# Kernel optimization log

Measured on AMD Instinct MI355X. Metric: run time of the kernel, lower is better.

Reference implementation:

```python
import jax, jax.numpy as jnp
import numpy as np

B, S, E, H = 2, 2048, 1024, 16
D = E // H  # head_dim = 64
SCALE = D ** -0.5
NEG = -1e9


def setup_inputs() -> dict:
    key = jax.random.key(0)
    ks = jax.random.split(key, 10)
    hidden_states = jax.random.normal(ks[0], (B, S, E), dtype=jnp.float32)
    # CLIP-style additive causal mask [B, 1, L, S]
    causal = jnp.where(jnp.tril(jnp.ones((S, S), dtype=bool)), 0.0, NEG).astype(jnp.float32)
    attn_mask = jnp.broadcast_to(causal, (B, 1, S, S))
    def lin(kw, kb):
        W = jax.random.normal(kw, (E, E), dtype=jnp.float32) * (E ** -0.5)
        b = jax.random.normal(kb, (E,), dtype=jnp.float32) * 0.02
        return W, b
    Wq, bq = lin(ks[1], ks[2])
    Wk, bk = lin(ks[3], ks[4])
    Wv, bv = lin(ks[5], ks[6])
    Wo, bo = lin(ks[7], ks[8])
    return {"hidden_states": hidden_states, "attn_mask": attn_mask,
            "Wq": Wq, "bq": bq, "Wk": Wk, "bk": bk,
            "Wv": Wv, "bv": bv, "Wo": Wo, "bo": bo}


def reference(hidden_states, attn_mask, Wq, bq, Wk, bk, Wv, bv, Wo, bo):
    b, L, e = hidden_states.shape
    # projections (nn.Linear: x @ W.T + b)
    def split_heads(x):
        return x.reshape(b, L, H, D).transpose(0, 2, 1, 3)  # [b,h,l,d]
    q = split_heads(hidden_states @ Wq.T + bq)
    k = split_heads(hidden_states @ Wk.T + bk)
    v = split_heads(hidden_states @ Wv.T + bv)
    # QK^T * scale + additive mask, softmax, AV (dropout_p = 0 in eval)
    scores = jnp.einsum('bhld,bhsd->bhls', q, k) * SCALE + attn_mask
    attn = jax.nn.softmax(scores, axis=-1)
    ctx = jnp.einsum('bhls,bhsd->bhld', attn, v)
    ctx = ctx.transpose(0, 2, 1, 3).reshape(b, L, e)
    return ctx @ Wo.T + bo
```

## Files before the change

### kernel.cpp

```cpp
#include <hip/hip_runtime.h>
#include <hip/hip_bf16.h>
#include <stdint.h>


typedef __hip_bfloat16 bf16;
typedef short bf16x8 __attribute__((ext_vector_type(8)));
typedef short bf16x4 __attribute__((ext_vector_type(4)));
typedef float f32x4 __attribute__((ext_vector_type(4)));

__device__ __forceinline__ f32x4 mfma16(bf16x8 a, bf16x8 b, f32x4 c) {
  return __builtin_amdgcn_mfma_f32_16x16x32_bf16(a, b, c, 0, 0, 0);
}

__device__ __forceinline__ f32x4 mfma_k16(bf16x4 a, bf16x4 b, f32x4 c) {
#if __has_builtin(__builtin_amdgcn_mfma_f32_16x16x16bf16_1k)
  return __builtin_amdgcn_mfma_f32_16x16x16bf16_1k(a, b, c, 0, 0, 0);
#else
  f32x4 d;
  asm volatile("v_mfma_f32_16x16x16_bf16 %0, %1, %2, %3\n\ts_nop 7\n\ts_nop 7"
               : "=v"(d)
               : "v"(a), "v"(b), "v"(c));
  return d;
#endif
}

__device__ __forceinline__ void async16(const void* g, void* l) {
  __builtin_amdgcn_global_load_lds((const __attribute__((address_space(1))) void*)g,
                                   (__attribute__((address_space(3))) void*)l, 16, 0, 0);
}

__global__ __launch_bounds__(256) void cvt_kernel(
    const float* __restrict__ hs, const float* __restrict__ Wq,
    const float* __restrict__ Wk, const float* __restrict__ Wv,
    const float* __restrict__ Wo, bf16* __restrict__ dst) {
  const size_t e = ((size_t)blockIdx.x * 256 + threadIdx.x) * 8;
  const float* src;
  size_t off;
  if (e < 4194304) {
    src = hs; off = e;
  } else {
    const size_t w = e - 4194304;
    const int wi = (int)(w >> 20);
    src = (wi == 0) ? Wq : (wi == 1) ? Wk : (wi == 2) ? Wv : Wo;
    off = w & 1048575;
  }
  const float4 a = *(const float4*)(src + off);
  const float4 b = *(const float4*)(src + off + 4);
  union { bf16 h[8]; uint4 u; } p;
  p.h[0] = __float2bfloat16(a.x); p.h[1] = __float2bfloat16(a.y);
  p.h[2] = __float2bfloat16(a.z); p.h[3] = __float2bfloat16(a.w);
  p.h[4] = __float2bfloat16(b.x); p.h[5] = __float2bfloat16(b.y);
  p.h[6] = __float2bfloat16(b.z); p.h[7] = __float2bfloat16(b.w);
  *(uint4*)(dst + e) = p.u;
}

__global__ __launch_bounds__(256, 3) void qkv_gemm(
    const bf16* __restrict__ X, const bf16* __restrict__ Wb,
    const float* __restrict__ bq, const float* __restrict__ bk,
    const float* __restrict__ bv, bf16* __restrict__ out) {
  constexpr int Kd = 1024;
  __shared__ bf16 sA[2][128 * 32];
  __shared__ bf16 sB[2][128 * 32];
  const int tid = threadIdx.x;
  const int wave = tid >> 6, lane = tid & 63;
  const int g = lane >> 4, ln = lane & 15;
  const int tM = blockIdx.y * 128, tN = blockIdx.x * 128;
  const int which = tN >> 10;
  const bf16* W = Wb + (size_t)which * 1048576;
  const float* bias = (which == 0) ? bq : (which == 1) ? bk : bv;
  const int tNl = tN & 1023;
  const float oscale = (which == 0) ? 0.18033688011112042f : 1.0f;
  const int wrow = (wave >> 1) * 64, wcol = (wave & 1) * 64;
  const f32x4 fz = {0.f, 0.f, 0.f, 0.f};

  f32x4 acc[4][4];
#pragma unroll
  for (int i = 0; i < 4; ++i)
#pragma unroll
    for (int j = 0; j < 4; ++j) acc[i][j] = fz;

  int srow[4], scol[4];
#pragma unroll
  for (int t = 0; t < 4; ++t) {
    const int d = tid + t * 256;
    srow[t] = (d >> 2) & 127;
    scol[t] = ((d >> 9) << 5) + ((d & 3) << 3);
  }

  for (int k0 = 0; k0 < Kd; k0 += 64) {
    __syncthreads();
#pragma unroll
    for (int t = 0; t < 4; ++t) {
      const int d = tid + t * 256;
      async16(X + (size_t)(tM + srow[t]) * Kd + k0 + scol[t], &sA[0][0] + d * 8);
      async16(W + (size_t)(tNl + srow[t]) * Kd + k0 + scol[t], &sB[0][0] + d * 8);
    }
    __syncthreads();
#pragma unroll
    for (int kk = 0; kk < 2; ++kk) {
      bf16x8 aF[4], bF[4];
#pragma unroll
      for (int i = 0; i < 4; ++i)
        aF[i] = *(const bf16x8*)(&sA[kk][0] + (wrow + i * 16 + ln) * 32 + g * 8);
#pragma unroll
      for (int j = 0; j < 4; ++j)
        bF[j] = *(const bf16x8*)(&sB[kk][0] + (wcol + j * 16 + ln) * 32 + g * 8);
#pragma unroll
      for (int i = 0; i < 4; ++i)
#pragma unroll
        for (int j = 0; j < 4; ++j) acc[i][j] = mfma16(aF[i], bF[j], acc[i][j]);
    }
  }

  bf16* outw = out + (size_t)which * 4194304;
  if (which == 2) {
    const int hh = (tNl + wcol) >> 6;
#pragma unroll
    for (int j = 0; j < 4; ++j) {
      const int nl = tNl + wcol + j * 16 + ln;
      const float bvf = bias[nl];
#pragma unroll
      for (int i = 0; i < 4; ++i) {
        const int m0 = tM + wrow + i * 16 + g * 4;
        const int b = m0 >> 11, t = (m0 & 2047) >> 6;
        union { bf16 hv[4]; bf16x4 v; } pk;
#pragma unroll
        for (int r = 0; r < 4; ++r) pk.hv[r] = __float2bfloat16(acc[i][j][r] + bvf);
        *(bf16x4*)(outw + (((size_t)(b * 16 + hh) * 32 + t) << 12) +
                   (i * 4 + j) * 256 + (g * 16 + ln) * 4) = pk.v;
      }
    }
  } else {
#pragma unroll
    for (int j = 0; j < 4; ++j) {
      const int nl = tNl + wcol + j * 16 + ln;
      const float bvf = bias[nl];
      const int h = nl >> 6, d = nl & 63;
#pragma unroll
      for (int i = 0; i < 4; ++i) {
#pragma unroll
        for (int r = 0; r < 4; ++r) {
          const int m = tM + wrow + i * 16 + g * 4 + r;
          const int b = m >> 11, s = m & 2047;
          const float v = (acc[i][j][r] + bvf) * oscale;
          outw[(((size_t)(b * 16 + h) * 2048 + s) << 6) + d] = __float2bfloat16(v);
        }
      }
    }
  }
}

__global__ __launch_bounds__(256, 4) void out_gemm(
    const bf16* __restrict__ X, const bf16* __restrict__ W,
    const float* __restrict__ bias, float* __restrict__ out) {
  constexpr int Kd = 1024;
  __shared__ bf16 sA[64 * 32];
  __shared__ bf16 sB[64 * 32];
  const int tid = threadIdx.x;
  const int wave = tid >> 6, lane = tid & 63;
  const int g = lane >> 4, ln = lane & 15;
  const int tM = blockIdx.y * 64, tN = blockIdx.x * 64;
  const f32x4 fz = {0.f, 0.f, 0.f, 0.f};

  f32x4 acc[4];
#pragma unroll
  for (int j = 0; j < 4; ++j) acc[j] = fz;

  const int srow = tid >> 2, scol = (tid & 3) << 3;
  for (int k0 = 0; k0 < Kd; k0 += 32) {
    __syncthreads();
    async16(X + (size_t)(tM + srow) * Kd + k0 + scol, sA + tid * 8);
    async16(W + (size_t)(tN + srow) * Kd + k0 + scol, sB + tid * 8);
    __syncthreads();
    const bf16x8 aF = *(const bf16x8*)(sA + (wave * 16 + ln) * 32 + g * 8);
    bf16x8 bF[4];
#pragma unroll
    for (int j = 0; j < 4; ++j)
      bF[j] = *(const bf16x8*)(sB + (j * 16 + ln) * 32 + g * 8);
#pragma unroll
    for (int j = 0; j < 4; ++j) acc[j] = mfma16(aF, bF[j], acc[j]);
  }

#pragma unroll
  for (int j = 0; j < 4; ++j) {
    const int n = tN + j * 16 + ln;
    const float bvf = bias[n];
#pragma unroll
    for (int r = 0; r < 4; ++r) {
      const int m = tM + wave * 16 + g * 4 + r;
      out[(size_t)m * 1024 + n] = acc[j][r] + bvf;
    }
  }
}

__global__ __launch_bounds__(256, 4) void attn_kernel(
    const bf16* __restrict__ Q, const bf16* __restrict__ K,
    const bf16* __restrict__ V, bf16* __restrict__ O) {
  constexpr int S = 2048, D = 64;
  __shared__ bf16 sK[64 * 72];
  __shared__ bf16 sVf[2][64 * 64];

  const int tid = threadIdx.x;
  const int w = tid >> 6, lane = tid & 63;
  const int g = lane >> 4, ln = lane & 15;
  const int px = blockIdx.x, py = blockIdx.y;
  const int bh = (px & 7) * 4 + (py & 3);
  const int s = py >> 3;
  const int q0 = (px >> 3) + 4 * ((py >> 2) & 1);
  const int qt = (s == 0) ? 31 - q0
               : (s == 1) ? 16 + q0
               : (s == 2) ? 15 - q0
                          : q0;
  const int b = bh >> 4, h = bh & 15;
  const f32x4 fz = {0.f, 0.f, 0.f, 0.f};

  const bf16* Qb = Q + (size_t)bh * S * D;
  const bf16* Kb = K + (size_t)bh * S * D;
  const bf16* Vfb = V + (size_t)bh * 131072;

  const int kr0 = tid >> 3, kc0 = (tid & 7) << 3;

  bf16x8 qf[2];
#pragma unroll
  for (int kc = 0; kc < 2; ++kc)
    qf[kc] = *(const bf16x8*)(Qb + (size_t)(qt * 64 + w * 16 + ln) * D + kc * 32 + g * 8);

  f32x4 oacc[4];
#pragma unroll
  for (int db = 0; db < 4; ++db) oacc[db] = fz;
  f32x4 lacc = fz;
  const short onebf = (short)0x3F80;
  const bf16x4 onesf = {onebf, onebf, onebf, onebf};

  uint4 kreg0 = *(const uint4*)(Kb + (size_t)kr0 * D + kc0);
  uint4 kreg1 = *(const uint4*)(Kb + (size_t)(kr0 + 32) * D + kc0);
  async16(Vfb + tid * 8, &sVf[0][0] + tid * 8);
  async16(Vfb + 2048 + tid * 8, &sVf[0][0] + 2048 + tid * 8);

  for (int kt = 0; kt <= qt; ++kt) {
    __syncthreads();
    *(uint4*)(sK + kr0 * 72 + kc0) = kreg0;
    *(uint4*)(sK + (kr0 + 32) * 72 + kc0) = kreg1;
    __syncthreads();
    if (kt < qt) {
      const bf16* vs = Vfb + (kt + 1) * 4096;
      bf16* vb = &sVf[(kt + 1) & 1][0];
      async16(vs + tid * 8, vb + tid * 8);
      async16(vs + 2048 + tid * 8, vb + 2048 + tid * 8);
      const size_t nb = (size_t)(kt + 1) * 64;
      kreg0 = *(const uint4*)(Kb + (nb + kr0) * D + kc0);
      kreg1 = *(const uint4*)(Kb + (nb + kr0 + 32) * D + kc0);
    }

    f32x4 sacc[4];
#pragma unroll
    for (int kb = 0; kb < 4; ++kb) sacc[kb] = fz;
#pragma unroll
    for (int kb = 0; kb < 4; ++kb) {
      const bf16x8 k0 = *(const bf16x8*)(sK + (kb * 16 + ln) * 72 + g * 8);
      const bf16x8 k1 = *(const bf16x8*)(sK + (kb * 16 + ln) * 72 + 32 + g * 8);
      sacc[kb] = mfma16(k0, qf[0], sacc[kb]);
      sacc[kb] = mfma16(k1, qf[1], sacc[kb]);
    }

    const bool diag = (kt == qt);
    const int qloc = w * 16 + ln;
    bf16x4 pa[4];
#pragma unroll
    for (int kb = 0; kb < 4; ++kb) {
      union { bf16 hh[4]; bf16x4 v; } pu;
#pragma unroll
      for (int r = 0; r < 4; ++r) {
        float pv = exp2f(sacc[kb][r]);
        if (diag && (kb * 16 + g * 4 + r > qloc)) pv = 0.f;
        pu.hh[r] = __float2bfloat16(pv);
      }
      pa[kb] = pu.v;
      lacc = mfma_k16(pa[kb], onesf, lacc);
    }

    const bf16* sVc = &sVf[kt & 1][0];
#pragma unroll
    for (int db = 0; db < 4; ++db) {
#pragma unroll
      for (int kb = 0; kb < 4; ++kb) {
        const bf16x4 vf =
            *(const bf16x4*)(sVc + ((kb * 4 + db) * 64 + g * 16 + ln) * 4);
        oacc[db] = mfma_k16(pa[kb], vf, oacc[db]);
      }
    }
  }

  float invl[4];
#pragma unroll
  for (int r = 0; r < 4; ++r) invl[r] = 1.0f / lacc[r];

#pragma unroll
  for (int db = 0; db < 4; ++db)
#pragma unroll
    for (int r = 0; r < 4; ++r) {
      const int row = qt * 64 + w * 16 + g * 4 + r;
      const int col = db * 16 + ln;
      O[(((size_t)(b * 2048 + row) * 16 + h) << 6) + col] =
          __float2bfloat16(oacc[db][r] * invl[r]);
    }
}

extern "C" void kernel_launch(void* const* d_in, const int* in_sizes, int n_in,
                              void* d_out, int out_size, void* d_ws, size_t ws_size,
                              hipStream_t stream) {
  const float* hs = (const float*)d_in[0];
  const float* Wq = (const float*)d_in[2];
  const float* bq = (const float*)d_in[3];
  const float* Wk = (const float*)d_in[4];
  const float* bk = (const float*)d_in[5];
  const float* Wv = (const float*)d_in[6];
  const float* bv = (const float*)d_in[7];
  const float* Wo = (const float*)d_in[8];
  const float* bo = (const float*)d_in[9];
  float* out = (float*)d_out;

  char* ws = (char*)d_ws;
  bf16* XW = (bf16*)ws;
  bf16* Xb = XW;
  bf16* W3b = XW + 4194304;
  bf16* Wob = XW + 7340032;
  bf16* Qw = (bf16*)(ws + (16u << 20));
  bf16* Kw = (bf16*)(ws + (24u << 20));
  bf16* Vw = (bf16*)(ws + (32u << 20));
  bf16* Cw = (bf16*)ws;

  const dim3 blk(256);
  cvt_kernel<<<4096, blk, 0, stream>>>(hs, Wq, Wk, Wv, Wo, XW);
  qkv_gemm<<<dim3(24, 32), blk, 0, stream>>>(Xb, W3b, bq, bk, bv, Qw);
  attn_kernel<<<dim3(32, 32), blk, 0, stream>>>(Qw, Kw, Vw, Cw);
  out_gemm<<<dim3(16, 64), blk, 0, stream>>>(Cw, Wob, bo, out);
}
```

Before: 194.8 us.

## Store K in MFMA fragment layout and double-buffer it via async LDS loads

The QKV GEMM epilogue now writes K per 64x64 tile in a pre-swizzled fragment order that matches the MFMA operand layout, as was already done for V. The attention kernel then loads K tiles with async global-to-LDS copies into a double buffer, instead of staging them through registers with padded rows. This removes one __syncthreads per iteration and the register round-trip, and gives contiguous conflict-free LDS reads. The cost is scattered 2-byte stores in the K epilogue and more LDS per block.

```diff
diff --git a/kernel.cpp b/kernel.cpp
--- a/kernel.cpp
+++ b/kernel.cpp
@@ -69,7 +69,6 @@
   const bf16* W = Wb + (size_t)which * 1048576;
   const float* bias = (which == 0) ? bq : (which == 1) ? bk : bv;
   const int tNl = tN & 1023;
-  const float oscale = (which == 0) ? 0.18033688011112042f : 1.0f;
   const int wrow = (wave >> 1) * 64, wcol = (wave & 1) * 64;
   const f32x4 fz = {0.f, 0.f, 0.f, 0.f};
 
@@ -130,7 +129,28 @@
                    (i * 4 + j) * 256 + (g * 16 + ln) * 4) = pk.v;
       }
     }
+  } else if (which == 1) {
+    const int hh = (tNl + wcol) >> 6;
+#pragma unroll
+    for (int j = 0; j < 4; ++j) {
+      const int nl = tNl + wcol + j * 16 + ln;
+      const float bvf = bias[nl];
+      const int half = j >> 1;
+      const int gg = (j * 2 + (ln >> 3)) & 3;
+      const int dl = ln & 7;
+#pragma unroll
+      for (int i = 0; i < 4; ++i) {
+        const int m0 = tM + wrow + i * 16 + g * 4;
+        const int b = m0 >> 11, t = (m0 & 2047) >> 6;
+        bf16* basep = outw + (((size_t)(b * 16 + hh) * 32 + t) << 12) +
+                      ((i * 2 + half) * 64 + gg * 16 + g * 4) * 8 + dl;
+#pragma unroll
+        for (int r = 0; r < 4; ++r)
+          basep[r * 8] = __float2bfloat16(acc[i][j][r] + bvf);
+      }
+    }
   } else {
+    const float oscale = 0.18033688011112042f;
 #pragma unroll
     for (int j = 0; j < 4; ++j) {
       const int nl = tNl + wcol + j * 16 + ln;
@@ -197,8 +217,8 @@
     const bf16* __restrict__ Q, const bf16* __restrict__ K,
     const bf16* __restrict__ V, bf16* __restrict__ O) {
   constexpr int S = 2048, D = 64;
-  __shared__ bf16 sK[64 * 72];
-  __shared__ bf16 sVf[2][64 * 64];
+  __shared__ bf16 sKf[2][4096];
+  __shared__ bf16 sVf[2][4096];
 
   const int tid = threadIdx.x;
   const int w = tid >> 6, lane = tid & 63;
@@ -215,10 +235,8 @@
   const f32x4 fz = {0.f, 0.f, 0.f, 0.f};
 
   const bf16* Qb = Q + (size_t)bh * S * D;
-  const bf16* Kb = K + (size_t)bh * S * D;
+  const bf16* Kfb = K + (size_t)bh * 131072;
   const bf16* Vfb = V + (size_t)bh * 131072;
-
-  const int kr0 = tid >> 3, kc0 = (tid & 7) << 3;
 
   bf16x8 qf[2];
 #pragma unroll
@@ -232,33 +250,33 @@
   const short onebf = (short)0x3F80;
   const bf16x4 onesf = {onebf, onebf, onebf, onebf};
 
-  uint4 kreg0 = *(const uint4*)(Kb + (size_t)kr0 * D + kc0);
-  uint4 kreg1 = *(const uint4*)(Kb + (size_t)(kr0 + 32) * D + kc0);
+  async16(Kfb + tid * 8, &sKf[0][0] + tid * 8);
+  async16(Kfb + 2048 + tid * 8, &sKf[0][0] + 2048 + tid * 8);
   async16(Vfb + tid * 8, &sVf[0][0] + tid * 8);
   async16(Vfb + 2048 + tid * 8, &sVf[0][0] + 2048 + tid * 8);
 
   for (int kt = 0; kt <= qt; ++kt) {
     __syncthreads();
-    *(uint4*)(sK + kr0 * 72 + kc0) = kreg0;
-    *(uint4*)(sK + (kr0 + 32) * 72 + kc0) = kreg1;
-    __syncthreads();
     if (kt < qt) {
-      const bf16* vs = Vfb + (kt + 1) * 4096;
-      bf16* vb = &sVf[(kt + 1) & 1][0];
-      async16(vs + tid * 8, vb + tid * 8);
-      async16(vs + 2048 + tid * 8, vb + 2048 + tid * 8);
-      const size_t nb = (size_t)(kt + 1) * 64;
-      kreg0 = *(const uint4*)(Kb + (nb + kr0) * D + kc0);
-      kreg1 = *(const uint4*)(Kb + (nb + kr0 + 32) * D + kc0);
-    }
+      const bf16* ks = Kfb + (size_t)(kt + 1) * 4096;
+      const bf16* vs = Vfb + (size_t)(kt + 1) * 4096;
+      bf16* kb_ = &sKf[(kt + 1) & 1][0];
+      bf16* vb_ = &sVf[(kt + 1) & 1][0];
+      async16(ks + tid * 8, kb_ + tid * 8);
+      async16(ks + 2048 + tid * 8, kb_ + 2048 + tid * 8);
+      async16(vs + tid * 8, vb_ + tid * 8);
+      async16(vs + 2048 + tid * 8, vb_ + 2048 + tid * 8);
+    }
+    const bf16* sKc = &sKf[kt & 1][0];
+    const bf16* sVc = &sVf[kt & 1][0];
 
     f32x4 sacc[4];
 #pragma unroll
     for (int kb = 0; kb < 4; ++kb) sacc[kb] = fz;
 #pragma unroll
     for (int kb = 0; kb < 4; ++kb) {
-      const bf16x8 k0 = *(const bf16x8*)(sK + (kb * 16 + ln) * 72 + g * 8);
-      const bf16x8 k1 = *(const bf16x8*)(sK + (kb * 16 + ln) * 72 + 32 + g * 8);
+      const bf16x8 k0 = *(const bf16x8*)(sKc + (kb * 2 + 0) * 512 + lane * 8);
+      const bf16x8 k1 = *(const bf16x8*)(sKc + (kb * 2 + 1) * 512 + lane * 8);
       sacc[kb] = mfma16(k0, qf[0], sacc[kb]);
       sacc[kb] = mfma16(k1, qf[1], sacc[kb]);
     }
@@ -279,7 +297,6 @@
       lacc = mfma_k16(pa[kb], onesf, lacc);
     }
 
-    const bf16* sVc = &sVf[kt & 1][0];
 #pragma unroll
     for (int db = 0; db < 4; ++db) {
 #pragma unroll
```

Measured after the change: 196.8 us. Within noise of the previous version (+1.0%).
